# Kernel tuning notes

Hardware: AMD Instinct MI355X
Metric: run time of the kernel (lower is better)

## Reference

```python
import jax, jax.numpy as jnp
import numpy as np

HIDDEN = 1024
NUM_HEADS = 16
HEAD_SIZE = HIDDEN // NUM_HEADS
B, S = 2, 2048


def setup_inputs() -> dict:
    key = jax.random.key(0)
    k_x, k_wqkv, k_bqkv, k_wo, k_bo = jax.random.split(key, 5)
    x = jax.random.normal(k_x, (B, S, HIDDEN), dtype=jnp.float32)
    # Dense kernels, fan-in scaled like lecun_normal init
    Wqkv = jax.random.normal(k_wqkv, (HIDDEN, 3 * HIDDEN), dtype=jnp.float32) / np.sqrt(HIDDEN)
    bqkv = jnp.zeros((3 * HIDDEN,), dtype=jnp.float32)
    Wo = jax.random.normal(k_wo, (HIDDEN, HIDDEN), dtype=jnp.float32) / np.sqrt(HIDDEN)
    bo = jnp.zeros((HIDDEN,), dtype=jnp.float32)
    return {"x": x, "Wqkv": Wqkv, "bqkv": bqkv, "Wo": Wo, "bo": bo}


def reference(x, Wqkv, bqkv, Wo, bo):
    b, s, h = x.shape
    qkv = jnp.einsum('bsh,hf->bsf', x, Wqkv) + bqkv          # [b, s, 3*h]
    qkv = qkv.reshape(b, s, 3, NUM_HEADS, HEAD_SIZE)
    q, k, v = qkv[:, :, 0], qkv[:, :, 1], qkv[:, :, 2]        # [b, s, nh, hd]
    scale = 1.0 / np.sqrt(HEAD_SIZE)
    scores = jnp.einsum('bqhd,bkhd->bhqk', q, k) * scale      # [b, nh, s, s]
    weights = jax.nn.softmax(scores, axis=-1)
    attn = jnp.einsum('bhqk,bkhd->bqhd', weights, v)          # [b, s, nh, hd]
    attn = attn.reshape(b, s, h)
    return jnp.einsum('bsh,hf->bsf', attn, Wo) + bo
```

## Files before the change

kernel.cpp:

```cpp
#include <hip/hip_runtime.h>
#include <hip/hip_bf16.h>

#define HIDDEN 1024
#define NH 16
#define BATCH 2
#define SEQ 2048

typedef __attribute__((ext_vector_type(8))) short bf16x8;
typedef __attribute__((ext_vector_type(4))) float f32x4;
typedef __attribute__((ext_vector_type(2))) uint uint2v;

__device__ __forceinline__ ushort f2bf(float f) {
    __hip_bfloat16 h = __float2bfloat16(f);
    return *reinterpret_cast<ushort*>(&h);
}
__device__ __forceinline__ float fexp2(float x) {
#if __has_builtin(__builtin_amdgcn_exp2f)
    return __builtin_amdgcn_exp2f(x);
#else
    return exp2f(x);
#endif
}
__device__ __forceinline__ uint pack_bf_trunc(float a, float b) {
    return __builtin_amdgcn_perm(__float_as_uint(b), __float_as_uint(a), 0x07060302u);
}

__device__ __forceinline__ void bfly(uint &a, uint &b) {
#if __has_builtin(__builtin_amdgcn_permlane16_swap)
    uint2v t = __builtin_amdgcn_permlane16_swap(a, b, false, false);
    uint2v s = __builtin_amdgcn_permlane32_swap(t[0], t[1], false, false);
    a = s[0]; b = s[1];
#else
    asm volatile("v_permlane16_swap_b32 %0, %1" : "+v"(a), "+v"(b));
    asm volatile("v_permlane32_swap_b32 %0, %1" : "+v"(a), "+v"(b));
#endif
}

__device__ __forceinline__ void async_copy16(const ushort* g, ushort* l) {
    __builtin_amdgcn_global_load_lds((const __attribute__((address_space(1))) void*)g,
                                     (__attribute__((address_space(3))) void*)l,
                                     16, 0, 0);
}

__global__ void prep_kernel(const float* __restrict__ x,
                            const float* __restrict__ Wqkv,
                            const float* __restrict__ Wo,
                            ushort* __restrict__ xb,
                            ushort* __restrict__ Wt,
                            ushort* __restrict__ WoT)
{
    __shared__ float t[32][33];
    const int bid = blockIdx.x;
    const int tid = threadIdx.x;

    if (bid < 4096) {
        int i = (bid * 256 + tid) * 4;
        float4 v = *(const float4*)(x + i);
        ushort4 w;
        w.x = f2bf(v.x); w.y = f2bf(v.y); w.z = f2bf(v.z); w.w = f2bf(v.w);
        *(ushort4*)(xb + i) = w;
        return;
    }
    const int r = tid >> 3;
    const int c = (tid & 7) * 4;
    if (bid < 7168) {
        int tt = bid - 4096;
        int k0 = (tt & 31) * 32;
        int n0 = (tt >> 5) * 32;
        const int N = 3 * HIDDEN, K = HIDDEN;
        float4 v = *(const float4*)(Wqkv + (size_t)(k0 + r) * N + n0 + c);
        t[r][c] = v.x; t[r][c + 1] = v.y; t[r][c + 2] = v.z; t[r][c + 3] = v.w;
        __syncthreads();
        ushort4 w;
        w.x = f2bf(t[c + 0][r]); w.y = f2bf(t[c + 1][r]);
        w.z = f2bf(t[c + 2][r]); w.w = f2bf(t[c + 3][r]);
        *(ushort4*)(Wt + (size_t)(n0 + r) * K + k0 + c) = w;
    } else {
        int tt = bid - 7168;
        int k0 = (tt & 31) * 32;
        int n0 = (tt >> 5) * 32;
        const int N = HIDDEN, K = HIDDEN;
        float4 v = *(const float4*)(Wo + (size_t)(k0 + r) * N + n0 + c);
        t[r][c] = v.x; t[r][c + 1] = v.y; t[r][c + 2] = v.z; t[r][c + 3] = v.w;
        __syncthreads();
        ushort4 w;
        w.x = f2bf(t[c + 0][r]); w.y = f2bf(t[c + 1][r]);
        w.z = f2bf(t[c + 2][r]); w.w = f2bf(t[c + 3][r]);
        *(ushort4*)(WoT + (size_t)(n0 + r) * K + k0 + c) = w;
    }
}

__global__ __launch_bounds__(256, 3)
void gemm_mfma_bf16_kernel(const ushort* __restrict__ A,
                           const ushort* __restrict__ Bt,
                           const float* __restrict__ bias,
                           ushort* __restrict__ C, int N,
                           int qscale_cols, float qscale,
                           ushort* __restrict__ vtg, int vt_mode)
{
    constexpr int K = 1024;
    __shared__ ushort As[128 * 64];
    __shared__ ushort Bs[128 * 64];

    const int tid  = threadIdx.x;
    const int wave = tid >> 6;
    const int lane = tid & 63;
    const int l16  = lane & 15;
    const int quad = lane >> 4;
    const int wm = wave & 1, wn = wave >> 1;

    const int bm = blockIdx.y * 128;
    const int bn = blockIdx.x * 128;

    const int srow = lane >> 3;
    const int lblk = (lane & 7) ^ srow;
    const ushort* Ag = A  + (size_t)(bm + wave * 32 + srow) * K + lblk * 8;
    const ushort* Bg = Bt + (size_t)(bn + wave * 32 + srow) * K + lblk * 8;
    ushort* Asl = As + wave * 32 * 64;
    ushort* Bsl = Bs + wave * 32 * 64;

    f32x4 acc[4][4];
    #pragma unroll
    for (int i = 0; i < 4; i++)
        #pragma unroll
        for (int j = 0; j < 4; j++) acc[i][j] = (f32x4){0.f, 0.f, 0.f, 0.f};

    for (int k0 = 0; k0 < K; k0 += 64) {
        __syncthreads();
        #pragma unroll
        for (int t = 0; t < 4; t++) {
            async_copy16(Ag + (size_t)t * 8 * K + k0, Asl + t * 8 * 64);
            async_copy16(Bg + (size_t)t * 8 * K + k0, Bsl + t * 8 * 64);
        }
        __syncthreads();

        #pragma unroll
        for (int s = 0; s < 2; s++) {
            bf16x8 af[4], bfr[4];
            #pragma unroll
            for (int i = 0; i < 4; i++) {
                int m = wm * 64 + i * 16 + l16;
                int n = wn * 64 + i * 16 + l16;
                af[i]  = *(const bf16x8*)&As[m * 64 + (((s * 4 + quad) ^ (m & 7)) << 3)];
                bfr[i] = *(const bf16x8*)&Bs[n * 64 + (((s * 4 + quad) ^ (n & 7)) << 3)];
            }
            #pragma unroll
            for (int i = 0; i < 4; i++)
                #pragma unroll
                for (int j = 0; j < 4; j++)
                    acc[i][j] = __builtin_amdgcn_mfma_f32_16x16x32_bf16(af[i], bfr[j], acc[i][j], 0, 0, 0);
        }
    }

    #pragma unroll
    for (int j = 0; j < 4; j++) {
        int col = bn + wn * 64 + j * 16 + l16;
        float bv = bias[col];
        if (vt_mode && col >= 2048) {
            int dfull = col - 2048;
            int hh = dfull >> 6, dd = dfull & 63;
            int bb = bm >> 11;
            int sb = ((bm & 2047) + wm * 64) >> 6;
            ushort tmp[16];
            #pragma unroll
            for (int i = 0; i < 4; i++)
                #pragma unroll
                for (int r = 0; r < 4; r++)
                    tmp[r * 4 + i] = f2bf(acc[i][j][r] + bv);
            ushort* dst = vtg + ((size_t)((bb * NH + hh) * 64 + dd)) * SEQ
                          + sb * 64 + quad * 16;
            *(uint4*)dst = *(const uint4*)tmp;
            *(uint4*)(dst + 8) = *(const uint4*)(tmp + 8);
        } else {
            float s = (col < qscale_cols) ? qscale : 1.0f;
            #pragma unroll
            for (int i = 0; i < 4; i++) {
                int row0 = bm + wm * 64 + i * 16 + quad * 4;
                #pragma unroll
                for (int r = 0; r < 4; r++)
                    C[(size_t)(row0 + r) * N + col] = f2bf((acc[i][j][r] + bv) * s);
            }
        }
    }
}

__global__ __launch_bounds__(256, 4)
void gemm_out_kernel(const ushort* __restrict__ A,
                     const ushort* __restrict__ Bt,
                     const float* __restrict__ bias,
                     float* __restrict__ C)
{
    constexpr int K = 1024, N = 1024;
    __shared__ ushort As[128 * 64];
    __shared__ ushort Bs[64 * 64];

    const int tid  = threadIdx.x;
    const int wave = tid >> 6;
    const int lane = tid & 63;
    const int l16  = lane & 15;
    const int quad = lane >> 4;
    const int wm = wave & 1, wn = wave >> 1;

    const int bm = blockIdx.y * 128;
    const int bn = blockIdx.x * 64;

    const int srow = lane >> 3;
    const int lblk = (lane & 7) ^ srow;
    const ushort* Ag = A  + (size_t)(bm + wave * 32 + srow) * K + lblk * 8;
    const ushort* Bg = Bt + (size_t)(bn + wave * 16 + srow) * K + lblk * 8;
    ushort* Asl = As + wave * 32 * 64;
    ushort* Bsl = Bs + wave * 16 * 64;

    f32x4 acc[4][2];
    #pragma unroll
    for (int i = 0; i < 4; i++)
        #pragma unroll
        for (int j = 0; j < 2; j++) acc[i][j] = (f32x4){0.f, 0.f, 0.f, 0.f};

    for (int k0 = 0; k0 < K; k0 += 64) {
        __syncthreads();
        #pragma unroll
        for (int t = 0; t < 4; t++)
            async_copy16(Ag + (size_t)t * 8 * K + k0, Asl + t * 8 * 64);
        #pragma unroll
        for (int t = 0; t < 2; t++)
            async_copy16(Bg + (size_t)t * 8 * K + k0, Bsl + t * 8 * 64);
        __syncthreads();

        #pragma unroll
        for (int s = 0; s < 2; s++) {
            bf16x8 af[4], bfr[2];
            #pragma unroll
            for (int i = 0; i < 4; i++) {
                int m = wm * 64 + i * 16 + l16;
                af[i] = *(const bf16x8*)&As[m * 64 + (((s * 4 + quad) ^ (m & 7)) << 3)];
            }
            #pragma unroll
            for (int j = 0; j < 2; j++) {
                int n = wn * 32 + j * 16 + l16;
                bfr[j] = *(const bf16x8*)&Bs[n * 64 + (((s * 4 + quad) ^ (n & 7)) << 3)];
            }
            #pragma unroll
            for (int i = 0; i < 4; i++)
                #pragma unroll
                for (int j = 0; j < 2; j++)
                    acc[i][j] = __builtin_amdgcn_mfma_f32_16x16x32_bf16(af[i], bfr[j], acc[i][j], 0, 0, 0);
        }
    }

    #pragma unroll
    for (int j = 0; j < 2; j++) {
        int col = bn + wn * 32 + j * 16 + l16;
        float bv = bias[col];
        #pragma unroll
        for (int i = 0; i < 4; i++) {
            int row0 = bm + wm * 64 + i * 16 + quad * 4;
            #pragma unroll
            for (int r = 0; r < 4; r++)
                C[(size_t)(row0 + r) * N + col] = acc[i][j][r] + bv;
        }
    }
}

__global__ __launch_bounds__(256, 2)
void attn_mfma_v12_kernel(const ushort* __restrict__ qkvb,
                          const ushort* __restrict__ vtg,
                          ushort* __restrict__ attn)
{
    __shared__ __align__(16) ushort smem[16384];

    const int tid  = threadIdx.x;
    const int wave = tid >> 6;
    const int lane = tid & 63;
    const int l16  = lane & 15;
    const int quad = lane >> 4;

    const int obid = blockIdx.x;
    const int qb = (obid >> 3) & 15;
    const int bh = (obid & 7) * 4 + (obid >> 7);
    const int h  = bh & (NH - 1);
    const int b  = bh >> 4;

    const int qbase = qb * 128 + wave * 32;
    const int hoff  = h * 64;

    bf16x8 a_q[2][2];
    #pragma unroll
    for (int mg = 0; mg < 2; mg++) {
        int qrow = b * SEQ + qbase + mg * 16 + l16;
        const ushort* qp = qkvb + (size_t)qrow * 3072 + hoff + quad * 8;
        a_q[mg][0] = *(const bf16x8*)qp;
        a_q[mg][1] = *(const bf16x8*)(qp + 32);
    }

    f32x4 o[2][4];
    f32x4 lacc[2];
    #pragma unroll
    for (int mg = 0; mg < 2; mg++) {
        lacc[mg] = (f32x4){0.f, 0.f, 0.f, 0.f};
        #pragma unroll
        for (int nt = 0; nt < 4; nt++) o[mg][nt] = (f32x4){0.f, 0.f, 0.f, 0.f};
    }

    bf16x8 b_ones;
    #pragma unroll
    for (int j = 0; j < 8; j++) b_ones[j] = (short)0x3f80;

    const ushort* kvb    = qkvb + (size_t)b * SEQ * 3072;
    const ushort* vtg_bh = vtg + (size_t)((b * NH + h) * 64) * SEQ;

    const int srow8 = lane >> 3;
    const int gblk  = ((lane & 7) ^ srow8) << 3;
    const ushort* kg = kvb + (size_t)(wave * 16 + srow8) * 3072 + 1024 + hoff + gblk;
    const ushort* vg = vtg_bh + (size_t)(wave * 16 + srow8) * SEQ + gblk;

    ushort* k_dst = smem + wave * 1024;
    ushort* v_dst = smem + 8192 + wave * 1024;

    #pragma unroll
    for (int c = 0; c < 2; c++) {
        async_copy16(kg + (size_t)(c * 8) * 3072, k_dst + c * 512);
        async_copy16(vg + (size_t)(c * 8) * SEQ,  v_dst + c * 512);
    }
    __syncthreads();

    int cur = 0;
    for (int t = 0; t < 32; t++) {
        if (t < 31) {
            const int k0n = (t + 1) * 64;
            #pragma unroll
            for (int c = 0; c < 2; c++) {
                async_copy16(kg + (size_t)(k0n + c * 8) * 3072,
                             k_dst + c * 512 + ((cur ^ 1) << 12));
                async_copy16(vg + (size_t)(c * 8) * SEQ + k0n,
                             v_dst + c * 512 + ((cur ^ 1) << 12));
            }
        }
        const ushort* Ks = smem + (cur << 12);
        const ushort* Vs = smem + 8192 + (cur << 12);

        f32x4 sc[2][4];
        __builtin_amdgcn_s_setprio(1);
        #pragma unroll
        for (int nt = 0; nt < 4; nt++) {
            int key = nt * 16 + l16;
            bf16x8 bk0 = *(const bf16x8*)&Ks[key * 64 + ((quad ^ (key & 7)) << 3)];
            bf16x8 bk1 = *(const bf16x8*)&Ks[key * 64 + (((4 + quad) ^ (key & 7)) << 3)];
            #pragma unroll
            for (int mg = 0; mg < 2; mg++) {
                f32x4 a = (f32x4){0.f, 0.f, 0.f, 0.f};
                a = __builtin_amdgcn_mfma_f32_16x16x32_bf16(bk0, a_q[mg][0], a, 0, 0, 0);
                a = __builtin_amdgcn_mfma_f32_16x16x32_bf16(bk1, a_q[mg][1], a, 0, 0, 0);
                sc[mg][nt] = a;
            }
        }
        __builtin_amdgcn_s_setprio(0);

        bf16x8 ap[2][2];
        #pragma unroll
        for (int mg = 0; mg < 2; mg++) {
            uint w00 = pack_bf_trunc(fexp2(sc[mg][0][0]), fexp2(sc[mg][1][0]));
            uint w01 = pack_bf_trunc(fexp2(sc[mg][0][1]), fexp2(sc[mg][1][1]));
            uint w02 = pack_bf_trunc(fexp2(sc[mg][0][2]), fexp2(sc[mg][1][2]));
            uint w03 = pack_bf_trunc(fexp2(sc[mg][0][3]), fexp2(sc[mg][1][3]));
            uint w10 = pack_bf_trunc(fexp2(sc[mg][2][0]), fexp2(sc[mg][3][0]));
            uint w11 = pack_bf_trunc(fexp2(sc[mg][2][1]), fexp2(sc[mg][3][1]));
            uint w12 = pack_bf_trunc(fexp2(sc[mg][2][2]), fexp2(sc[mg][3][2]));
            uint w13 = pack_bf_trunc(fexp2(sc[mg][2][3]), fexp2(sc[mg][3][3]));
            bfly(w00, w02);
            bfly(w01, w03);
            bfly(w10, w12);
            bfly(w11, w13);
            union { uint u[4]; bf16x8 h; } u0, u1;
            u0.u[0] = w00; u0.u[1] = w10; u0.u[2] = w01; u0.u[3] = w11;
            u1.u[0] = w02; u1.u[1] = w12; u1.u[2] = w03; u1.u[3] = w13;
            ap[mg][0] = u0.h;
            ap[mg][1] = u1.h;
        }

        __builtin_amdgcn_s_setprio(1);
        #pragma unroll
        for (int nt = 0; nt < 4; nt++) {
            int d = nt * 16 + l16;
            bf16x8 bv0 = *(const bf16x8*)&Vs[d * 64 + ((quad ^ (d & 7)) << 3)];
            bf16x8 bv1 = *(const bf16x8*)&Vs[d * 64 + (((4 + quad) ^ (d & 7)) << 3)];
            #pragma unroll
            for (int mg = 0; mg < 2; mg++) {
                o[mg][nt] = __builtin_amdgcn_mfma_f32_16x16x32_bf16(ap[mg][0], bv0, o[mg][nt], 0, 0, 0);
                o[mg][nt] = __builtin_amdgcn_mfma_f32_16x16x32_bf16(ap[mg][1], bv1, o[mg][nt], 0, 0, 0);
            }
        }
        #pragma unroll
        for (int mg = 0; mg < 2; mg++) {
            lacc[mg] = __builtin_amdgcn_mfma_f32_16x16x32_bf16(ap[mg][0], b_ones, lacc[mg], 0, 0, 0);
            lacc[mg] = __builtin_amdgcn_mfma_f32_16x16x32_bf16(ap[mg][1], b_ones, lacc[mg], 0, 0, 0);
        }
        __builtin_amdgcn_s_setprio(0);

        __syncthreads();
        cur ^= 1;
    }

    #pragma unroll
    for (int mg = 0; mg < 2; mg++) {
        #pragma unroll
        for (int r = 0; r < 4; r++) {
            float inv = 1.f / lacc[mg][r];
            int row = b * SEQ + qbase + mg * 16 + quad * 4 + r;
            size_t base = (size_t)row * HIDDEN + hoff + l16;
            #pragma unroll
            for (int nt = 0; nt < 4; nt++)
                attn[base + nt * 16] = f2bf(o[mg][nt][r] * inv);
        }
    }
}

__global__ __launch_bounds__(512, 4)
void attn_mfma_fb_kernel(const ushort* __restrict__ qkvb,
                         ushort* __restrict__ attn)
{
    __shared__ __align__(16) ushort smem[34816];

    const int tid   = threadIdx.x;
    const int wave  = tid >> 6;
    const int wavel = wave & 3;
    const int kh    = wave >> 2;
    const int lane  = tid & 63;
    const int l16   = lane & 15;
    const int quad  = lane >> 4;

    const int qb = blockIdx.x & 15;
    const int bh = blockIdx.x >> 4;
    const int h  = bh & (NH - 1);
    const int b  = bh >> 4;

    const int qbase = qb * 128;
    const int hoff  = h * 64;

    ushort* KsH = smem + kh * 4096;
    ushort* VsH = smem + 8192 + kh * 4096;
    ushort* Psw = smem + 16384 + wave * 2304;

    bf16x8 a_q[2][2];
    #pragma unroll
    for (int mg = 0; mg < 2; mg++) {
        int qrow = b * SEQ + qbase + wavel * 32 + mg * 16 + l16;
        const ushort* qp = qkvb + (size_t)qrow * 3072 + hoff + quad * 8;
        a_q[mg][0] = *(const bf16x8*)qp;
        a_q[mg][1] = *(const bf16x8*)(qp + 32);
    }

    f32x4 o[2][4];
    f32x4 lacc[2];
    #pragma unroll
    for (int mg = 0; mg < 2; mg++) {
        lacc[mg] = (f32x4){0.f, 0.f, 0.f, 0.f};
        #pragma unroll
        for (int nt = 0; nt < 4; nt++) o[mg][nt] = (f32x4){0.f, 0.f, 0.f, 0.f};
    }

    bf16x8 b_ones;
    #pragma unroll
    for (int j = 0; j < 8; j++) b_ones[j] = (short)0x3f80;

    const ushort* kvb = qkvb + (size_t)b * SEQ * 3072;

    for (int t = 0; t < 16; t++) {
        const int k0 = t * 64;
        __syncthreads();
        {
            const int tl = tid & 255;
            #pragma unroll
            for (int i = 0; i < 2; i++) {
                int key = (tl >> 3) + 32 * i;
                int blk = tl & 7;
                const ushort* ksrc = kvb + (size_t)(kh * 1024 + k0 + key) * 3072 + 1024 + hoff + blk * 8;
                uint4 kv = *(const uint4*)ksrc;
                *(uint4*)&KsH[key * 64 + ((blk ^ (key & 7)) << 3)] = kv;
                uint4 vv = *(const uint4*)(ksrc + 1024);
                const ushort* vpp = (const ushort*)&vv;
                int pk_ = (key & 15) * 4 + (key >> 4);
                #pragma unroll
                for (int j = 0; j < 8; j++) {
                    int d = blk * 8 + j;
                    VsH[d * 64 + (((pk_ >> 3) ^ (d & 7)) << 3) + (pk_ & 7)] = vpp[j];
                }
            }
        }
        __syncthreads();

        f32x4 sc[2][4];
        #pragma unroll
        for (int nt = 0; nt < 4; nt++) {
            int key = nt * 16 + l16;
            bf16x8 bk0 = *(const bf16x8*)&KsH[key * 64 + ((quad ^ (key & 7)) << 3)];
            bf16x8 bk1 = *(const bf16x8*)&KsH[key * 64 + (((4 + quad) ^ (key & 7)) << 3)];
            #pragma unroll
            for (int mg = 0; mg < 2; mg++) {
                f32x4 a = (f32x4){0.f, 0.f, 0.f, 0.f};
                a = __builtin_amdgcn_mfma_f32_16x16x32_bf16(a_q[mg][0], bk0, a, 0, 0, 0);
                a = __builtin_amdgcn_mfma_f32_16x16x32_bf16(a_q[mg][1], bk1, a, 0, 0, 0);
                sc[mg][nt] = a;
            }
        }

        #pragma unroll
        for (int mg = 0; mg < 2; mg++) {
            #pragma unroll
            for (int r = 0; r < 4; r++) {
                int q = mg * 16 + quad * 4 + r;
                uint2 pk2;
                pk2.x = pack_bf_trunc(fexp2(sc[mg][0][r]), fexp2(sc[mg][1][r]));
                pk2.y = pack_bf_trunc(fexp2(sc[mg][2][r]), fexp2(sc[mg][3][r]));
                *(uint2*)&Psw[q * 72 + l16 * 4] = pk2;
            }
        }

        asm volatile("s_waitcnt lgkmcnt(0)" ::: "memory");
        bf16x8 a_p[2][2];
        #pragma unroll
        for (int mg = 0; mg < 2; mg++) {
            a_p[mg][0] = *(const bf16x8*)&Psw[(mg * 16 + l16) * 72 + quad * 8];
            a_p[mg][1] = *(const bf16x8*)&Psw[(mg * 16 + l16) * 72 + 32 + quad * 8];
        }

        #pragma unroll
        for (int nt = 0; nt < 4; nt++) {
            int d = nt * 16 + l16;
            bf16x8 bv0 = *(const bf16x8*)&VsH[d * 64 + ((quad ^ (d & 7)) << 3)];
            bf16x8 bv1 = *(const bf16x8*)&VsH[d * 64 + (((4 + quad) ^ (d & 7)) << 3)];
            #pragma unroll
            for (int mg = 0; mg < 2; mg++) {
                o[mg][nt] = __builtin_amdgcn_mfma_f32_16x16x32_bf16(a_p[mg][0], bv0, o[mg][nt], 0, 0, 0);
                o[mg][nt] = __builtin_amdgcn_mfma_f32_16x16x32_bf16(a_p[mg][1], bv1, o[mg][nt], 0, 0, 0);
            }
        }
        #pragma unroll
        for (int mg = 0; mg < 2; mg++) {
            lacc[mg] = __builtin_amdgcn_mfma_f32_16x16x32_bf16(a_p[mg][0], b_ones, lacc[mg], 0, 0, 0);
            lacc[mg] = __builtin_amdgcn_mfma_f32_16x16x32_bf16(a_p[mg][1], b_ones, lacc[mg], 0, 0, 0);
        }
    }

    __syncthreads();
    float* osc = (float*)smem;
    float* lsc = (float*)(smem + 16384);
    const int fo = wavel * 2048 + quad * 64 + l16 * 4;
    const int fl = wavel * 512 + quad * 64 + l16 * 4;
    if (kh == 1) {
        #pragma unroll
        for (int mg = 0; mg < 2; mg++) {
            #pragma unroll
            for (int nt = 0; nt < 4; nt++)
                *(f32x4*)&osc[fo + (mg * 4 + nt) * 256] = o[mg][nt];
            *(f32x4*)&lsc[fl + mg * 256] = lacc[mg];
        }
    }
    __syncthreads();
    if (kh == 0) {
        #pragma unroll
        for (int mg = 0; mg < 2; mg++) {
            #pragma unroll
            for (int nt = 0; nt < 4; nt++)
                o[mg][nt] += *(const f32x4*)&osc[fo + (mg * 4 + nt) * 256];
            lacc[mg] += *(const f32x4*)&lsc[fl + mg * 256];
        }
        #pragma unroll
        for (int mg = 0; mg < 2; mg++) {
            #pragma unroll
            for (int r = 0; r < 4; r++) {
                float inv = 1.f / lacc[mg][r];
                int row = b * SEQ + qbase + wavel * 32 + mg * 16 + quad * 4 + r;
                size_t base = (size_t)row * HIDDEN + hoff + l16;
                #pragma unroll
                for (int nt = 0; nt < 4; nt++)
                    attn[base + nt * 16] = f2bf(o[mg][nt][r] * inv);
            }
        }
    }
}

extern "C" void kernel_launch(void* const* d_in, const int* in_sizes, int n_in,
                              void* d_out, int out_size, void* d_ws, size_t ws_size,
                              hipStream_t stream) {
    const float* x    = (const float*)d_in[0];
    const float* Wqkv = (const float*)d_in[1];
    const float* bqkv = (const float*)d_in[2];
    const float* Wo   = (const float*)d_in[3];
    const float* bo   = (const float*)d_in[4];
    float* out = (float*)d_out;

    const int M = BATCH * SEQ;
    const size_t MB = 1024 * 1024;

    char* ws = (char*)d_ws;
    ushort* qkvb = (ushort*)ws;
    ushort* attn = (ushort*)(ws + 24 * MB);
    ushort* xb   = (ushort*)(ws + 24 * MB);
    ushort* Wt   = (ushort*)(ws + 32 * MB);
    ushort* WoT  = (ushort*)(ws + 38 * MB);
    ushort* vtg  = (ushort*)(ws + 40 * MB);
    const int use_vtg = (ws_size >= 48 * MB) ? 1 : 0;

    const float qscale = 0.125f * 1.44269504088896f;

    prep_kernel<<<8192, 256, 0, stream>>>(x, Wqkv, Wo, xb, Wt, WoT);

    {
        dim3 grid((3 * HIDDEN) / 128, M / 128);
        gemm_mfma_bf16_kernel<<<grid, 256, 0, stream>>>(xb, Wt, bqkv, qkvb,
                                                        3 * HIDDEN, HIDDEN, qscale,
                                                        vtg, use_vtg);
    }

    if (use_vtg) {
        attn_mfma_v12_kernel<<<BATCH * NH * (SEQ / 128), 256, 0, stream>>>(
            qkvb, vtg, attn);
    } else {
        attn_mfma_fb_kernel<<<BATCH * NH * (SEQ / 128), 512, 0, stream>>>(
            qkvb, attn);
    }

    {
        dim3 grid(HIDDEN / 64, M / 128);
        gemm_out_kernel<<<grid, 256, 0, stream>>>(attn, WoT, bo, out);
    }
}
```

Baseline: 174.2 us.

## Double K/V tile to 128 keys per barrier and split prefetch issue

The attention kernel now stages 128 keys per pipeline stage (two 64-key subtiles) instead of 64, which halves the number of __syncthreads barriers over the sequence loop. Prefetch for K is issued before the first subtile and V prefetch after it, spreading global-to-LDS traffic across the compute. LDS use doubles to 64 KB per block, which may limit occupancy at 2 blocks per CU.

Result: no change. 174.9 us (+0.4%).

```diff
diff --git a/kernel.cpp b/kernel.cpp
--- a/kernel.cpp
+++ b/kernel.cpp
@@ -262,12 +262,76 @@
     }
 }
 
+__device__ __forceinline__ void attn_tile64(
+    const ushort* Ks, const ushort* Vs,
+    const bf16x8 (&a_q)[2][2], f32x4 (&o)[2][4], f32x4 (&lacc)[2],
+    const bf16x8 &b_ones, int l16, int quad)
+{
+    f32x4 sc[2][4];
+    __builtin_amdgcn_s_setprio(1);
+    #pragma unroll
+    for (int nt = 0; nt < 4; nt++) {
+        int key = nt * 16 + l16;
+        bf16x8 bk0 = *(const bf16x8*)&Ks[key * 64 + ((quad ^ (key & 7)) << 3)];
+        bf16x8 bk1 = *(const bf16x8*)&Ks[key * 64 + (((4 + quad) ^ (key & 7)) << 3)];
+        #pragma unroll
+        for (int mg = 0; mg < 2; mg++) {
+            f32x4 a = (f32x4){0.f, 0.f, 0.f, 0.f};
+            a = __builtin_amdgcn_mfma_f32_16x16x32_bf16(bk0, a_q[mg][0], a, 0, 0, 0);
+            a = __builtin_amdgcn_mfma_f32_16x16x32_bf16(bk1, a_q[mg][1], a, 0, 0, 0);
+            sc[mg][nt] = a;
+        }
+    }
+    __builtin_amdgcn_s_setprio(0);
+
+    bf16x8 ap[2][2];
+    #pragma unroll
+    for (int mg = 0; mg < 2; mg++) {
+        uint w00 = pack_bf_trunc(fexp2(sc[mg][0][0]), fexp2(sc[mg][1][0]));
+        uint w01 = pack_bf_trunc(fexp2(sc[mg][0][1]), fexp2(sc[mg][1][1]));
+        uint w02 = pack_bf_trunc(fexp2(sc[mg][0][2]), fexp2(sc[mg][1][2]));
+        uint w03 = pack_bf_trunc(fexp2(sc[mg][0][3]), fexp2(sc[mg][1][3]));
+        uint w10 = pack_bf_trunc(fexp2(sc[mg][2][0]), fexp2(sc[mg][3][0]));
+        uint w11 = pack_bf_trunc(fexp2(sc[mg][2][1]), fexp2(sc[mg][3][1]));
+        uint w12 = pack_bf_trunc(fexp2(sc[mg][2][2]), fexp2(sc[mg][3][2]));
+        uint w13 = pack_bf_trunc(fexp2(sc[mg][2][3]), fexp2(sc[mg][3][3]));
+        bfly(w00, w02);
+        bfly(w01, w03);
+        bfly(w10, w12);
+        bfly(w11, w13);
+        union { uint u[4]; bf16x8 h; } u0, u1;
+        u0.u[0] = w00; u0.u[1] = w10; u0.u[2] = w01; u0.u[3] = w11;
+        u1.u[0] = w02; u1.u[1] = w12; u1.u[2] = w03; u1.u[3] = w13;
+        ap[mg][0] = u0.h;
+        ap[mg][1] = u1.h;
+    }
+
+    __builtin_amdgcn_s_setprio(1);
+    #pragma unroll
+    for (int nt = 0; nt < 4; nt++) {
+        int d = nt * 16 + l16;
+        bf16x8 bv0 = *(const bf16x8*)&Vs[d * 64 + ((quad ^ (d & 7)) << 3)];
+        bf16x8 bv1 = *(const bf16x8*)&Vs[d * 64 + (((4 + quad) ^ (d & 7)) << 3)];
+        #pragma unroll
+        for (int mg = 0; mg < 2; mg++) {
+            o[mg][nt] = __builtin_amdgcn_mfma_f32_16x16x32_bf16(ap[mg][0], bv0, o[mg][nt], 0, 0, 0);
+            o[mg][nt] = __builtin_amdgcn_mfma_f32_16x16x32_bf16(ap[mg][1], bv1, o[mg][nt], 0, 0, 0);
+        }
+    }
+    #pragma unroll
+    for (int mg = 0; mg < 2; mg++) {
+        lacc[mg] = __builtin_amdgcn_mfma_f32_16x16x32_bf16(ap[mg][0], b_ones, lacc[mg], 0, 0, 0);
+        lacc[mg] = __builtin_amdgcn_mfma_f32_16x16x32_bf16(ap[mg][1], b_ones, lacc[mg], 0, 0, 0);
+    }
+    __builtin_amdgcn_s_setprio(0);
+}
+
 __global__ __launch_bounds__(256, 2)
-void attn_mfma_v12_kernel(const ushort* __restrict__ qkvb,
+void attn_mfma_v13_kernel(const ushort* __restrict__ qkvb,
                           const ushort* __restrict__ vtg,
                           ushort* __restrict__ attn)
 {
-    __shared__ __align__(16) ushort smem[16384];
+    __shared__ __align__(16) ushort smem[32768];
 
     const int tid  = threadIdx.x;
     const int wave = tid >> 6;
@@ -315,87 +379,48 @@
     const ushort* vg = vtg_bh + (size_t)(wave * 16 + srow8) * SEQ + gblk;
 
     ushort* k_dst = smem + wave * 1024;
-    ushort* v_dst = smem + 8192 + wave * 1024;
-
-    #pragma unroll
-    for (int c = 0; c < 2; c++) {
-        async_copy16(kg + (size_t)(c * 8) * 3072, k_dst + c * 512);
-        async_copy16(vg + (size_t)(c * 8) * SEQ,  v_dst + c * 512);
-    }
+    ushort* v_dst = smem + 16384 + wave * 1024;
+
+    #pragma unroll
+    for (int s = 0; s < 2; s++)
+        #pragma unroll
+        for (int c = 0; c < 2; c++) {
+            async_copy16(kg + (size_t)(s * 64 + c * 8) * 3072,
+                         k_dst + s * 4096 + c * 512);
+            async_copy16(vg + (size_t)(c * 8) * SEQ + s * 64,
+                         v_dst + s * 4096 + c * 512);
+        }
     __syncthreads();
 
     int cur = 0;
-    for (int t = 0; t < 32; t++) {
-        if (t < 31) {
-            const int k0n = (t + 1) * 64;
-            #pragma unroll
-            for (int c = 0; c < 2; c++) {
-                async_copy16(kg + (size_t)(k0n + c * 8) * 3072,
-                             k_dst + c * 512 + ((cur ^ 1) << 12));
-                async_copy16(vg + (size_t)(c * 8) * SEQ + k0n,
-                             v_dst + c * 512 + ((cur ^ 1) << 12));
-            }
-        }
-        const ushort* Ks = smem + (cur << 12);
-        const ushort* Vs = smem + 8192 + (cur << 12);
-
-        f32x4 sc[2][4];
-        __builtin_amdgcn_s_setprio(1);
-        #pragma unroll
-        for (int nt = 0; nt < 4; nt++) {
-            int key = nt * 16 + l16;
-            bf16x8 bk0 = *(const bf16x8*)&Ks[key * 64 + ((quad ^ (key & 7)) << 3)];
-            bf16x8 bk1 = *(const bf16x8*)&Ks[key * 64 + (((4 + quad) ^ (key & 7)) << 3)];
-            #pragma unroll
-            for (int mg = 0; mg < 2; mg++) {
-                f32x4 a = (f32x4){0.f, 0.f, 0.f, 0.f};
-                a = __builtin_amdgcn_mfma_f32_16x16x32_bf16(bk0, a_q[mg][0], a, 0, 0, 0);
-                a = __builtin_amdgcn_mfma_f32_16x16x32_bf16(bk1, a_q[mg][1], a, 0, 0, 0);
-                sc[mg][nt] = a;
-            }
-        }
-        __builtin_amdgcn_s_setprio(0);
-
-        bf16x8 ap[2][2];
-        #pragma unroll
-        for (int mg = 0; mg < 2; mg++) {
-            uint w00 = pack_bf_trunc(fexp2(sc[mg][0][0]), fexp2(sc[mg][1][0]));
-            uint w01 = pack_bf_trunc(fexp2(sc[mg][0][1]), fexp2(sc[mg][1][1]));
-            uint w02 = pack_bf_trunc(fexp2(sc[mg][0][2]), fexp2(sc[mg][1][2]));
-            uint w03 = pack_bf_trunc(fexp2(sc[mg][0][3]), fexp2(sc[mg][1][3]));
-            uint w10 = pack_bf_trunc(fexp2(sc[mg][2][0]), fexp2(sc[mg][3][0]));
-            uint w11 = pack_bf_trunc(fexp2(sc[mg][2][1]), fexp2(sc[mg][3][1]));
-            uint w12 = pack_bf_trunc(fexp2(sc[mg][2][2]), fexp2(sc[mg][3][2]));
-            uint w13 = pack_bf_trunc(fexp2(sc[mg][2][3]), fexp2(sc[mg][3][3]));
-            bfly(w00, w02);
-            bfly(w01, w03);
-            bfly(w10, w12);
-            bfly(w11, w13);
-            union { uint u[4]; bf16x8 h; } u0, u1;
-            u0.u[0] = w00; u0.u[1] = w10; u0.u[2] = w01; u0.u[3] = w11;
-            u1.u[0] = w02; u1.u[1] = w12; u1.u[2] = w03; u1.u[3] = w13;
-            ap[mg][0] = u0.h;
-            ap[mg][1] = u1.h;
-        }
-
-        __builtin_amdgcn_s_setprio(1);
-        #pragma unroll
-        for (int nt = 0; nt < 4; nt++) {
-            int d = nt * 16 + l16;
-            bf16x8 bv0 = *(const bf16x8*)&Vs[d * 64 + ((quad ^ (d & 7)) << 3)];
-            bf16x8 bv1 = *(const bf16x8*)&Vs[d * 64 + (((4 + quad) ^ (d & 7)) << 3)];
-            #pragma unroll
-            for (int mg = 0; mg < 2; mg++) {
-                o[mg][nt] = __builtin_amdgcn_mfma_f32_16x16x32_bf16(ap[mg][0], bv0, o[mg][nt], 0, 0, 0);
-                o[mg][nt] = __builtin_amdgcn_mfma_f32_16x16x32_bf16(ap[mg][1], bv1, o[mg][nt], 0, 0, 0);
-            }
-        }
-        #pragma unroll
-        for (int mg = 0; mg < 2; mg++) {
-            lacc[mg] = __builtin_amdgcn_mfma_f32_16x16x32_bf16(ap[mg][0], b_ones, lacc[mg], 0, 0, 0);
-            lacc[mg] = __builtin_amdgcn_mfma_f32_16x16x32_bf16(ap[mg][1], b_ones, lacc[mg], 0, 0, 0);
-        }
-        __builtin_amdgcn_s_setprio(0);
+    for (int t = 0; t < 16; t++) {
+        const int nb = (cur ^ 1) << 13;
+        if (t < 15) {
+            const int k0n = (t + 1) * 128;
+            #pragma unroll
+            for (int s = 0; s < 2; s++)
+                #pragma unroll
+                for (int c = 0; c < 2; c++)
+                    async_copy16(kg + (size_t)(k0n + s * 64 + c * 8) * 3072,
+                                 k_dst + nb + s * 4096 + c * 512);
+        }
+
+        const ushort* Kc = smem + (cur << 13);
+        const ushort* Vc = smem + 16384 + (cur << 13);
+
+        attn_tile64(Kc, Vc, a_q, o, lacc, b_ones, l16, quad);
+
+        if (t < 15) {
+            const int k0n = (t + 1) * 128;
+            #pragma unroll
+            for (int s = 0; s < 2; s++)
+                #pragma unroll
+                for (int c = 0; c < 2; c++)
+                    async_copy16(vg + (size_t)(c * 8) * SEQ + k0n + s * 64,
+                                 v_dst + nb + s * 4096 + c * 512);
+        }
+
+        attn_tile64(Kc + 4096, Vc + 4096, a_q, o, lacc, b_ones, l16, quad);
 
         __syncthreads();
         cur ^= 1;
@@ -614,7 +639,7 @@
     }
 
     if (use_vtg) {
-        attn_mfma_v12_kernel<<<BATCH * NH * (SEQ / 128), 256, 0, stream>>>(
+        attn_mfma_v13_kernel<<<BATCH * NH * (SEQ / 128), 256, 0, stream>>>(
             qkvb, vtg, attn);
     } else {
         attn_mfma_fb_kernel<<<BATCH * NH * (SEQ / 128), 512, 0, stream>>>(
```
